# Kernel optimization log

Measured on AMD Instinct MI355X. Metric: run time of the kernel, lower is better.

## Reference

```python
import jax, jax.numpy as jnp
import numpy as np
from itertools import combinations

Nt, Nrf, Nk, FEAT, BATCH = 64, 4, 8, 512, 1024
Ng = Nt // Nk                      # 8
_MAX = len(list(combinations(range(Ng), Nrf)))  # 70
CSETSIZE = int(2 ** np.floor(np.log2(_MAX)))    # 64
SQRT_NRF = np.float32(np.sqrt(Nrf))


def _generate_antenna_selection_set(num_target):
    """Max-hamming-distance antenna selection set (numpy, matches torch code)."""
    combs = list(combinations(range(Ng), Nrf))
    maxSize = len(combs)
    globalSet = np.zeros((maxSize, Nt, Nrf), np.float32)
    for i, act in enumerate(combs):
        for j, a in enumerate(act):
            globalSet[i, a * Nk:a * Nk + Nk, j] = 1.0
    gsum = globalSet.sum(-1)  # (maxSize, Nt)
    selectSet = np.zeros((num_target, Nt, Nrf), np.float32)
    available = []
    for idx in range(num_target):
        if len(available) == 0:
            available = list(range(maxSize))
        if idx == 0:
            hd = np.zeros(len(available))
        else:
            sel = selectSet[:idx].sum(-1)            # (idx, Nt)
            cand = gsum[np.array(available)]          # (nAvail, Nt)
            hd = (sel[None, :, :] != cand[:, None, :]).sum(axis=(1, 2))
        sid = available[int(np.argmax(hd))]
        selectSet[idx] = globalSet[sid]
        available.remove(sid)
    return selectSet


def setup_inputs() -> dict:
    key = jax.random.key(0)
    ks = jax.random.split(key, 7)
    s = 1.0 / np.sqrt(FEAT)
    DDIM = CSETSIZE * Nrf * Nrf
    return {
        "x": jax.random.normal(ks[0], (BATCH, FEAT), jnp.float32),
        "W_A": jax.random.normal(ks[1], (Nt, FEAT), jnp.float32) * s,
        "b_A": jax.random.normal(ks[2], (Nt,), jnp.float32) * s,
        "W_Dr": jax.random.normal(ks[3], (DDIM, FEAT), jnp.float32) * s,
        "b_Dr": jax.random.normal(ks[4], (DDIM,), jnp.float32) * s,
        "W_Di": jax.random.normal(ks[5], (DDIM, FEAT), jnp.float32) * s,
        "b_Di": jax.random.normal(ks[6], (DDIM,), jnp.float32) * s,
        "CSet": jnp.asarray(_generate_antenna_selection_set(CSETSIZE)),
    }


def reference(x, W_A, b_A, W_Dr, b_Dr, W_Di, b_Di, CSet):
    B = x.shape[0]
    theta = x @ W_A.T + b_A                          # (B, Nt)
    cosT, sinT = jnp.cos(theta), jnp.sin(theta)
    eye = jnp.eye(Nt, dtype=x.dtype)
    A_real = (cosT[:, :, None] * eye)[:, None]       # (B, 1, Nt, Nt) diag-embed
    A_imag = (sinT[:, :, None] * eye)[:, None]
    D_real = (x @ W_Dr.T + b_Dr).reshape(B, CSETSIZE, Nrf, Nrf)
    D_imag = (x @ W_Di.T + b_Di).reshape(B, CSETSIZE, Nrf, Nrf)
    # diag(cos) @ C == row-scale of C (identical math to the dense matmul)
    ArC = cosT[:, None, :, None] * CSet[None]        # (B, CSetSize, Nt, Nrf)
    AiC = sinT[:, None, :, None] * CSet[None]
    ArCDr = ArC @ D_real
    ArCDi = ArC @ D_imag
    AiCDr = AiC @ D_real
    AiCDi = AiC @ D_imag
    V_real = ArCDr - AiCDi                           # (B, CSetSize, Nt, Nrf)
    V_imag = ArCDi + AiCDr
    V_F = jnp.sqrt(jnp.sum(V_real ** 2 + V_imag ** 2, axis=(2, 3)))
    V_F = V_F[:, :, None, None]
    D_real_n = SQRT_NRF * D_real / V_F
    D_imag_n = SQRT_NRF * D_imag / V_F
    return (A_real, A_imag, D_real_n, D_imag_n, CSet)
```

## Files before the change

kernel.cpp:

```cpp
#include <hip/hip_runtime.h>
#include <math.h>

#define BATCH 1024
#define FEAT  512
#define NT    64
#define DDIM  1024

typedef __attribute__((ext_vector_type(8))) short  short8;
typedef __attribute__((ext_vector_type(4))) float  floatx4;

#define AIMG_OFF  0
#define BIMG_OFF  1048576
#define THETA_OFF 3276800

__device__ __forceinline__ unsigned short bf16rne(float f) {
    unsigned int u = __float_as_uint(f);
    return (unsigned short)((u + 0x7fffu + ((u >> 16) & 1u)) >> 16);
}

__device__ __forceinline__ void gld16(const unsigned char* g, unsigned char* l) {
    __builtin_amdgcn_global_load_lds(
        (const __attribute__((address_space(1))) unsigned int*)g,
        (__attribute__((address_space(3))) unsigned int*)l, 16, 0, 0);
}

__global__ __launch_bounds__(256) void k0_convert(
    const float* __restrict__ x,
    const float* __restrict__ W_A,
    const float* __restrict__ W_Dr,
    const float* __restrict__ W_Di,
    unsigned char* __restrict__ ws)
{
    unsigned short* aimg = (unsigned short*)(ws + AIMG_OFF);
    unsigned short* bimg = (unsigned short*)(ws + BIMG_OFF);
    const int gtid = blockIdx.x * 256 + threadIdx.x;

    for (int idx = gtid; idx < 200704; idx += 65536) {
        const float* src;
        unsigned short* dst;
        if (idx < 65536) {
            const int rt = idx >> 12, kb = (idx >> 9) & 7;
            const int r  = (idx >> 3) & 63, c = idx & 7;
            src = x + ((size_t)(rt * 64 + r) * FEAT + kb * 64 + c * 8);
            dst = aimg + ((rt * 8 + kb) * 4096 + r * 64 + ((c ^ (r & 7)) * 8));
        } else {
            const int j  = idx - 65536;
            const int ct = j >> 12, kb = (j >> 9) & 7;
            const int n  = (j >> 3) & 63, c = j & 7;
            const float* wrow;
            if (ct < 32) {
                const int g = n >> 5, h = (n >> 4) & 1, pos = n & 15;
                wrow = (h ? W_Di : W_Dr) + (size_t)(ct * 32 + g * 16 + pos) * FEAT;
            } else {
                wrow = W_A + (size_t)n * FEAT;
            }
            src = wrow + kb * 64 + c * 8;
            dst = bimg + ((ct * 8 + kb) * 4096 + n * 64 + ((c ^ (n & 7)) * 8));
        }
        const float4 v0 = *(const float4*)src;
        const float4 v1 = *(const float4*)(src + 4);
        short8 o;
        o[0] = (short)bf16rne(v0.x); o[1] = (short)bf16rne(v0.y);
        o[2] = (short)bf16rne(v0.z); o[3] = (short)bf16rne(v0.w);
        o[4] = (short)bf16rne(v1.x); o[5] = (short)bf16rne(v1.y);
        o[6] = (short)bf16rne(v1.z); o[7] = (short)bf16rne(v1.w);
        *(short8*)dst = o;
    }
}

__global__ __launch_bounds__(256) void k1_gemm(
    const unsigned char* __restrict__ ws,
    const float* __restrict__ b_A,
    const float* __restrict__ b_Dr, const float* __restrict__ b_Di,
    float* __restrict__ out, float* __restrict__ theta_ws)
{
    __shared__ __align__(16) unsigned char smem[32768];

    const int bid  = blockIdx.x;
    const int rt   = bid & 15;
    const int ct   = bid >> 4;
    const int tid  = threadIdx.x;
    const int lane = tid & 63;
    const int wv   = tid >> 6;
    const int ln   = lane & 15;
    const int quad = lane >> 4;
    const int row0 = rt * 64;

    const unsigned char* Atiles = ws + AIMG_OFF + (size_t)rt * 8 * 8192;
    const unsigned char* Btiles = ws + BIMG_OFF + (size_t)ct * 8 * 8192;

    const int g0 = (wv * 2 + 0) * 1024;
    const int g1 = (wv * 2 + 1) * 1024;
    const int lo = lane * 16;

    floatx4 acc[4] = {{0,0,0,0},{0,0,0,0},{0,0,0,0},{0,0,0,0}};

    {
        unsigned char* La = smem;
        unsigned char* Lb = smem + 8192;
        gld16(Atiles + g0 + lo, La + g0);
        gld16(Atiles + g1 + lo, La + g1);
        gld16(Btiles + g0 + lo, Lb + g0);
        gld16(Btiles + g1 + lo, Lb + g1);
    }

    const int rowOffA = (wv * 16 + ln) * 128;
    const int swz = ln & 7;
    int cur = 0;

    #pragma unroll 1
    for (int kb = 0; kb < 8; ++kb) {
        __syncthreads();
        if (kb < 7) {
            const unsigned char* At = Atiles + (kb + 1) * 8192;
            const unsigned char* Bt = Btiles + (kb + 1) * 8192;
            unsigned char* La = smem + (cur ^ 1) * 16384;
            unsigned char* Lb = La + 8192;
            gld16(At + g0 + lo, La + g0);
            gld16(At + g1 + lo, La + g1);
            gld16(Bt + g0 + lo, Lb + g0);
            gld16(Bt + g1 + lo, Lb + g1);
        }
        const unsigned char* La = smem + cur * 16384;
        const unsigned char* Lb = La + 8192;
        #pragma unroll
        for (int ks = 0; ks < 2; ++ks) {
            const int ca = ((ks * 4 + quad) ^ swz) * 16;
            const short8 a = *(const short8*)(La + rowOffA + ca);
            #pragma unroll
            for (int t = 0; t < 4; ++t) {
                const short8 b = *(const short8*)(Lb + (t * 16 + ln) * 128 + ca);
                acc[t] = __builtin_amdgcn_mfma_f32_16x16x32_bf16(a, b, acc[t], 0, 0, 0);
            }
        }
        cur ^= 1;
    }

    if (ct < 32) {
        const size_t drn = (size_t)2 * BATCH * 4096;
        const size_t din = drn + (size_t)BATCH * DDIM;
        const int woff = ct * 32;
        #pragma unroll
        for (int p = 0; p < 2; ++p) {
            const int colg = woff + p * 16 + ln;
            const float br = b_Dr[colg];
            const float bi = b_Di[colg];
            float dr[4], di[4], ps[4];
            #pragma unroll
            for (int i = 0; i < 4; ++i) {
                dr[i] = acc[2 * p][i] + br;
                di[i] = acc[2 * p + 1][i] + bi;
                ps[i] = dr[i] * dr[i] + di[i] * di[i];
            }
            #pragma unroll
            for (int i = 0; i < 4; ++i) {
                ps[i] += __shfl_xor(ps[i], 1);
                ps[i] += __shfl_xor(ps[i], 2);
                ps[i] += __shfl_xor(ps[i], 4);
                ps[i] += __shfl_xor(ps[i], 8);
            }
            #pragma unroll
            for (int i = 0; i < 4; ++i) {
                const float scale = 2.0f / sqrtf(8.0f * ps[i]);
                const size_t row_g = (size_t)(row0 + wv * 16 + quad * 4 + i);
                out[drn + row_g * DDIM + colg] = dr[i] * scale;
                out[din + row_g * DDIM + colg] = di[i] * scale;
            }
        }
    } else {
        #pragma unroll
        for (int t = 0; t < 4; ++t) {
            const int colg = t * 16 + ln;
            const float ba = b_A[colg];
            #pragma unroll
            for (int i = 0; i < 4; ++i) {
                const int row_g = row0 + wv * 16 + quad * 4 + i;
                theta_ws[row_g * NT + colg] = acc[t][i] + ba;
            }
        }
    }
}

__global__ __launch_bounds__(256) void k2_fill(
    const float* __restrict__ theta_ws,
    const float* __restrict__ cset,
    float* __restrict__ out)
{
    const int beta = blockIdx.x;
    const int tid  = threadIdx.x;

    if (beta < 4096) {
        const int b  = beta >> 2;
        const int rg = beta & 3;
        const int t  = rg * 16 + (tid >> 4);
        const int j  = tid & 15;

        const float th = theta_ws[b * NT + t];
        float s, c;
        sincosf(th, &s, &c);

        float4 vr = {0.f, 0.f, 0.f, 0.f};
        float4 vi = {0.f, 0.f, 0.f, 0.f};
        if ((t >> 2) == j) {
            ((float*)&vr)[t & 3] = c;
            ((float*)&vi)[t & 3] = s;
        }
        const size_t off = (size_t)b * 4096 + t * 64 + j * 4;
        *(float4*)(out + off) = vr;
        *(float4*)(out + (size_t)BATCH * 4096 + off) = vi;
    } else {
        const int cb = beta - 4096;
        const size_t base = (size_t)2 * BATCH * 4096 + (size_t)2 * BATCH * DDIM;
        ((float4*)(out + base))[cb * 256 + tid] = ((const float4*)cset)[cb * 256 + tid];
    }
}

extern "C" void kernel_launch(void* const* d_in, const int* in_sizes, int n_in,
                              void* d_out, int out_size, void* d_ws, size_t ws_size,
                              hipStream_t stream) {
    const float* x    = (const float*)d_in[0];
    const float* W_A  = (const float*)d_in[1];
    const float* b_A  = (const float*)d_in[2];
    const float* W_Dr = (const float*)d_in[3];
    const float* b_Dr = (const float*)d_in[4];
    const float* W_Di = (const float*)d_in[5];
    const float* b_Di = (const float*)d_in[6];
    const float* CSet = (const float*)d_in[7];
    float* out = (float*)d_out;
    unsigned char* ws = (unsigned char*)d_ws;
    float* theta = (float*)(ws + THETA_OFF);

    k0_convert<<<256, 256, 0, stream>>>(x, W_A, W_Dr, W_Di, ws);
    k1_gemm<<<528, 256, 0, stream>>>(ws, b_A, b_Dr, b_Di, out, theta);
    k2_fill<<<4112, 256, 0, stream>>>(theta, CSet, out);
}
```

Measured before the change: 108.4 us.

## Fuse theta computation and diag fill into conversion kernel, drop third launch

Computes theta = x·W_A^T + b_A directly in fp32 inside the first kernel, alongside the bf16 conversion and CSet copy, and writes the diagonal cos/sin outputs there. The GEMM kernel drops the W_A column tile and the theta workspace round trip, and the separate fill kernel is removed. This cuts one launch and the serialization between the GEMM and the large fill writes, at the cost of redundant fp32 dot products reading x and W_A per block.

```diff
diff --git a/kernel.cpp b/kernel.cpp
--- a/kernel.cpp
+++ b/kernel.cpp
@@ -11,7 +11,6 @@
 
 #define AIMG_OFF  0
 #define BIMG_OFF  1048576
-#define THETA_OFF 3276800
 
 __device__ __forceinline__ unsigned short bf16rne(float f) {
     unsigned int u = __float_as_uint(f);
@@ -24,55 +23,101 @@
         (__attribute__((address_space(3))) unsigned int*)l, 16, 0, 0);
 }
 
-__global__ __launch_bounds__(256) void k0_convert(
+__global__ __launch_bounds__(256) void k0_fused(
     const float* __restrict__ x,
     const float* __restrict__ W_A,
+    const float* __restrict__ b_A,
     const float* __restrict__ W_Dr,
     const float* __restrict__ W_Di,
-    unsigned char* __restrict__ ws)
+    const float* __restrict__ cset,
+    unsigned char* __restrict__ ws,
+    float* __restrict__ out)
 {
-    unsigned short* aimg = (unsigned short*)(ws + AIMG_OFF);
-    unsigned short* bimg = (unsigned short*)(ws + BIMG_OFF);
-    const int gtid = blockIdx.x * 256 + threadIdx.x;
-
-    for (int idx = gtid; idx < 200704; idx += 65536) {
-        const float* src;
-        unsigned short* dst;
-        if (idx < 65536) {
-            const int rt = idx >> 12, kb = (idx >> 9) & 7;
-            const int r  = (idx >> 3) & 63, c = idx & 7;
-            src = x + ((size_t)(rt * 64 + r) * FEAT + kb * 64 + c * 8);
-            dst = aimg + ((rt * 8 + kb) * 4096 + r * 64 + ((c ^ (r & 7)) * 8));
-        } else {
-            const int j  = idx - 65536;
-            const int ct = j >> 12, kb = (j >> 9) & 7;
-            const int n  = (j >> 3) & 63, c = j & 7;
-            const float* wrow;
-            if (ct < 32) {
+    const int beta = blockIdx.x;
+    const int tid  = threadIdx.x;
+
+    if (beta < 256) {
+        unsigned short* aimg = (unsigned short*)(ws + AIMG_OFF);
+        unsigned short* bimg = (unsigned short*)(ws + BIMG_OFF);
+        const int gtid = beta * 256 + tid;
+        #pragma unroll
+        for (int v = 0; v < 3; ++v) {
+            const int idx = gtid + v * 65536;
+            const float* src;
+            unsigned short* dst;
+            if (idx < 65536) {
+                const int rt = idx >> 12, kb = (idx >> 9) & 7;
+                const int r  = (idx >> 3) & 63, c = idx & 7;
+                src = x + ((size_t)(rt * 64 + r) * FEAT + kb * 64 + c * 8);
+                dst = aimg + ((rt * 8 + kb) * 4096 + r * 64 + ((c ^ (r & 7)) * 8));
+            } else {
+                const int j  = idx - 65536;
+                const int ct = j >> 12, kb = (j >> 9) & 7;
+                const int n  = (j >> 3) & 63, c = j & 7;
                 const int g = n >> 5, h = (n >> 4) & 1, pos = n & 15;
-                wrow = (h ? W_Di : W_Dr) + (size_t)(ct * 32 + g * 16 + pos) * FEAT;
-            } else {
-                wrow = W_A + (size_t)n * FEAT;
+                const float* wrow =
+                    (h ? W_Di : W_Dr) + (size_t)(ct * 32 + g * 16 + pos) * FEAT;
+                src = wrow + kb * 64 + c * 8;
+                dst = bimg + ((ct * 8 + kb) * 4096 + n * 64 + ((c ^ (n & 7)) * 8));
             }
-            src = wrow + kb * 64 + c * 8;
-            dst = bimg + ((ct * 8 + kb) * 4096 + n * 64 + ((c ^ (n & 7)) * 8));
-        }
-        const float4 v0 = *(const float4*)src;
-        const float4 v1 = *(const float4*)(src + 4);
-        short8 o;
-        o[0] = (short)bf16rne(v0.x); o[1] = (short)bf16rne(v0.y);
-        o[2] = (short)bf16rne(v0.z); o[3] = (short)bf16rne(v0.w);
-        o[4] = (short)bf16rne(v1.x); o[5] = (short)bf16rne(v1.y);
-        o[6] = (short)bf16rne(v1.z); o[7] = (short)bf16rne(v1.w);
-        *(short8*)dst = o;
+            const float4 v0 = *(const float4*)src;
+            const float4 v1 = *(const float4*)(src + 4);
+            short8 o;
+            o[0] = (short)bf16rne(v0.x); o[1] = (short)bf16rne(v0.y);
+            o[2] = (short)bf16rne(v0.z); o[3] = (short)bf16rne(v0.w);
+            o[4] = (short)bf16rne(v1.x); o[5] = (short)bf16rne(v1.y);
+            o[6] = (short)bf16rne(v1.z); o[7] = (short)bf16rne(v1.w);
+            *(short8*)dst = o;
+        }
+    } else if (beta < 4352) {
+        const int fb = beta - 256;
+        const int b  = fb >> 2;
+        const int rg = fb & 3;
+        const int tl = tid >> 4;
+        const int j  = tid & 15;
+        const int t  = rg * 16 + tl;
+
+        const float* xr = x   + (size_t)b * FEAT + j * 4;
+        const float* wr = W_A + (size_t)t * FEAT + j * 4;
+        float4 a = {0.f, 0.f, 0.f, 0.f};
+        #pragma unroll
+        for (int it = 0; it < 8; ++it) {
+            const float4 xv = *(const float4*)(xr + it * 64);
+            const float4 wv = *(const float4*)(wr + it * 64);
+            a.x = fmaf(xv.x, wv.x, a.x);
+            a.y = fmaf(xv.y, wv.y, a.y);
+            a.z = fmaf(xv.z, wv.z, a.z);
+            a.w = fmaf(xv.w, wv.w, a.w);
+        }
+        float th = (a.x + a.y) + (a.z + a.w);
+        th += __shfl_xor(th, 1);
+        th += __shfl_xor(th, 2);
+        th += __shfl_xor(th, 4);
+        th += __shfl_xor(th, 8);
+        th += b_A[t];
+
+        float4 vr = {0.f, 0.f, 0.f, 0.f};
+        float4 vi = {0.f, 0.f, 0.f, 0.f};
+        if ((t >> 2) == j) {
+            float s, c;
+            sincosf(th, &s, &c);
+            ((float*)&vr)[t & 3] = c;
+            ((float*)&vi)[t & 3] = s;
+        }
+        const size_t off = (size_t)b * 4096 + t * 64 + j * 4;
+        *(float4*)(out + off) = vr;
+        *(float4*)(out + (size_t)BATCH * 4096 + off) = vi;
+    } else {
+        const int cb = beta - 4352;
+        const size_t base = (size_t)2 * BATCH * 4096 + (size_t)2 * BATCH * DDIM;
+        ((float4*)(out + base))[cb * 256 + tid] = ((const float4*)cset)[cb * 256 + tid];
     }
 }
 
 __global__ __launch_bounds__(256) void k1_gemm(
     const unsigned char* __restrict__ ws,
-    const float* __restrict__ b_A,
     const float* __restrict__ b_Dr, const float* __restrict__ b_Di,
-    float* __restrict__ out, float* __restrict__ theta_ws)
+    float* __restrict__ out)
 {
     __shared__ __align__(16) unsigned char smem[32768];
 
@@ -136,82 +181,35 @@
         cur ^= 1;
     }
 
-    if (ct < 32) {
-        const size_t drn = (size_t)2 * BATCH * 4096;
-        const size_t din = drn + (size_t)BATCH * DDIM;
-        const int woff = ct * 32;
-        #pragma unroll
-        for (int p = 0; p < 2; ++p) {
-            const int colg = woff + p * 16 + ln;
-            const float br = b_Dr[colg];
-            const float bi = b_Di[colg];
-            float dr[4], di[4], ps[4];
-            #pragma unroll
-            for (int i = 0; i < 4; ++i) {
-                dr[i] = acc[2 * p][i] + br;
-                di[i] = acc[2 * p + 1][i] + bi;
-                ps[i] = dr[i] * dr[i] + di[i] * di[i];
-            }
-            #pragma unroll
-            for (int i = 0; i < 4; ++i) {
-                ps[i] += __shfl_xor(ps[i], 1);
-                ps[i] += __shfl_xor(ps[i], 2);
-                ps[i] += __shfl_xor(ps[i], 4);
-                ps[i] += __shfl_xor(ps[i], 8);
-            }
-            #pragma unroll
-            for (int i = 0; i < 4; ++i) {
-                const float scale = 2.0f / sqrtf(8.0f * ps[i]);
-                const size_t row_g = (size_t)(row0 + wv * 16 + quad * 4 + i);
-                out[drn + row_g * DDIM + colg] = dr[i] * scale;
-                out[din + row_g * DDIM + colg] = di[i] * scale;
-            }
-        }
-    } else {
-        #pragma unroll
-        for (int t = 0; t < 4; ++t) {
-            const int colg = t * 16 + ln;
-            const float ba = b_A[colg];
-            #pragma unroll
-            for (int i = 0; i < 4; ++i) {
-                const int row_g = row0 + wv * 16 + quad * 4 + i;
-                theta_ws[row_g * NT + colg] = acc[t][i] + ba;
-            }
-        }
-    }
-}
-
-__global__ __launch_bounds__(256) void k2_fill(
-    const float* __restrict__ theta_ws,
-    const float* __restrict__ cset,
-    float* __restrict__ out)
-{
-    const int beta = blockIdx.x;
-    const int tid  = threadIdx.x;
-
-    if (beta < 4096) {
-        const int b  = beta >> 2;
-        const int rg = beta & 3;
-        const int t  = rg * 16 + (tid >> 4);
-        const int j  = tid & 15;
-
-        const float th = theta_ws[b * NT + t];
-        float s, c;
-        sincosf(th, &s, &c);
-
-        float4 vr = {0.f, 0.f, 0.f, 0.f};
-        float4 vi = {0.f, 0.f, 0.f, 0.f};
-        if ((t >> 2) == j) {
-            ((float*)&vr)[t & 3] = c;
-            ((float*)&vi)[t & 3] = s;
-        }
-        const size_t off = (size_t)b * 4096 + t * 64 + j * 4;
-        *(float4*)(out + off) = vr;
-        *(float4*)(out + (size_t)BATCH * 4096 + off) = vi;
-    } else {
-        const int cb = beta - 4096;
-        const size_t base = (size_t)2 * BATCH * 4096 + (size_t)2 * BATCH * DDIM;
-        ((float4*)(out + base))[cb * 256 + tid] = ((const float4*)cset)[cb * 256 + tid];
+    const size_t drn = (size_t)2 * BATCH * 4096;
+    const size_t din = drn + (size_t)BATCH * DDIM;
+    const int woff = ct * 32;
+    #pragma unroll
+    for (int p = 0; p < 2; ++p) {
+        const int colg = woff + p * 16 + ln;
+        const float br = b_Dr[colg];
+        const float bi = b_Di[colg];
+        float dr[4], di[4], ps[4];
+        #pragma unroll
+        for (int i = 0; i < 4; ++i) {
+            dr[i] = acc[2 * p][i] + br;
+            di[i] = acc[2 * p + 1][i] + bi;
+            ps[i] = dr[i] * dr[i] + di[i] * di[i];
+        }
+        #pragma unroll
+        for (int i = 0; i < 4; ++i) {
+            ps[i] += __shfl_xor(ps[i], 1);
+            ps[i] += __shfl_xor(ps[i], 2);
+            ps[i] += __shfl_xor(ps[i], 4);
+            ps[i] += __shfl_xor(ps[i], 8);
+        }
+        #pragma unroll
+        for (int i = 0; i < 4; ++i) {
+            const float scale = 2.0f / sqrtf(8.0f * ps[i]);
+            const size_t row_g = (size_t)(row0 + wv * 16 + quad * 4 + i);
+            out[drn + row_g * DDIM + colg] = dr[i] * scale;
+            out[din + row_g * DDIM + colg] = di[i] * scale;
+        }
     }
 }
 
@@ -228,9 +226,7 @@
     const float* CSet = (const float*)d_in[7];
     float* out = (float*)d_out;
     unsigned char* ws = (unsigned char*)d_ws;
-    float* theta = (float*)(ws + THETA_OFF);
-
-    k0_convert<<<256, 256, 0, stream>>>(x, W_A, W_Dr, W_Di, ws);
-    k1_gemm<<<528, 256, 0, stream>>>(ws, b_A, b_Dr, b_Di, out, theta);
-    k2_fill<<<4112, 256, 0, stream>>>(theta, CSet, out);
-}
+
+    k0_fused<<<4368, 256, 0, stream>>>(x, W_A, b_A, W_Dr, W_Di, CSet, ws, out);
+    k1_gemm<<<512, 256, 0, stream>>>(ws, b_Dr, b_Di, out);
+}
```

Result: no change. 109.9 us (+1.4%).
